# Kernel tuning notes

Measured on AMD Instinct MI355X. Metric: run time of the kernel, lower is better.

## Reference

```python
import jax, jax.numpy as jnp
import numpy as np


def setup_inputs() -> dict:
    key = jax.random.key(0)
    ks = jax.random.split(key, 12)
    B, T, D, H = 256, 512, 128, 256
    s = 0.01
    inp = {
        "x": jax.random.normal(ks[0], (B, T, D), dtype=jnp.float32),
        "h_decay": jax.random.uniform(ks[1], (B, T), dtype=jnp.float32),
        "Wr": jax.random.normal(ks[2], (D, H), dtype=jnp.float32) * s,
        "Wz": jax.random.normal(ks[3], (D, H), dtype=jnp.float32) * s,
        "Wh": jax.random.normal(ks[4], (D, H), dtype=jnp.float32) * s,
        "Ur": jax.random.normal(ks[5], (H, H), dtype=jnp.float32) * s,
        "Uz": jax.random.normal(ks[6], (H, H), dtype=jnp.float32) * s,
        "Uh": jax.random.normal(ks[7], (H, H), dtype=jnp.float32) * s,
        "br": jax.random.normal(ks[8], (H,), dtype=jnp.float32) * s,
        "bz": jax.random.normal(ks[9], (H,), dtype=jnp.float32) * s,
        "bh": jax.random.normal(ks[10], (H,), dtype=jnp.float32) * s,
    }
    return inp


def reference(x, h_decay, Wr, Wz, Wh, Ur, Uz, Uh, br, bz, bh):
    B, T, D = x.shape
    H = Ur.shape[0]
    # Precompute input projections for all timesteps (same math, batched GEMM).
    xz = jnp.einsum("btd,dh->bth", x, Wz) + bz  # [B,T,H]
    xr = jnp.einsum("btd,dh->bth", x, Wr) + br
    xh = jnp.einsum("btd,dh->bth", x, Wh) + bh

    def step(h_tm1, inputs):
        xz_t, xr_t, xh_t, dec_t = inputs
        h_dec = dec_t[:, None] * h_tm1              # decay previous state
        z_t = jax.nn.sigmoid(xz_t + h_dec @ Uz)
        r_t = jax.nn.sigmoid(xr_t + h_dec @ Ur)
        h_prop = jnp.tanh(xh_t + (r_t * h_dec) @ Uh)
        h_t = (1.0 - z_t) * h_dec + z_t * h_prop
        return h_t, h_t

    h0 = jnp.zeros((B, H), dtype=x.dtype)
    scan_inputs = (
        jnp.swapaxes(xz, 0, 1),  # [T,B,H]
        jnp.swapaxes(xr, 0, 1),
        jnp.swapaxes(xh, 0, 1),
        jnp.swapaxes(h_decay, 0, 1),  # [T,B]
    )
    _, hs = jax.lax.scan(step, h0, scan_inputs)
    return jnp.swapaxes(hs, 0, 1)  # [B,T,H]
```

## Files before the change

### kernel.cpp

```cpp
#include <hip/hip_runtime.h>
#include <hip/hip_bf16.h>


static constexpr int Bb = 256;
static constexpr int Tt = 512;
static constexpr int Dd = 128;
static constexpr int Hh = 256;

typedef _Float16 half2_t __attribute__((ext_vector_type(2)));

__device__ __forceinline__ float dot2f(unsigned a, unsigned b, float c) {
  half2_t av, bv;
  __builtin_memcpy(&av, &a, 4);
  __builtin_memcpy(&bv, &b, 4);
#if __has_builtin(__builtin_amdgcn_fdot2)
  return __builtin_amdgcn_fdot2(av, bv, c, false);
#else
  return fmaf((float)av[1], (float)bv[1], fmaf((float)av[0], (float)bv[0], c));
#endif
}

__device__ __forceinline__ unsigned packh2(float lo, float hi) {
  half2_t hv;
  hv[0] = (_Float16)lo;
  hv[1] = (_Float16)hi;
  unsigned u;
  __builtin_memcpy(&u, &hv, 4);
  return u;
}

__global__ __launch_bounds__(256) void proj3_kernel(
    const float* __restrict__ x,
    const float* __restrict__ Wz, const float* __restrict__ Wr,
    const float* __restrict__ Wh,
    const float* __restrict__ bz, const float* __restrict__ br,
    const float* __restrict__ bh,
    float* __restrict__ oz, float* __restrict__ orr, float* __restrict__ oh)
{
  __shared__ unsigned xP[64][64];
  __shared__ unsigned wP[8][256];

  const int tid = threadIdx.x;
  const int ty = tid >> 5;
  const int tx = tid & 31;
  const size_t brow = (size_t)blockIdx.x * 64;

  #pragma unroll
  for (int it = 0; it < 8; ++it) {
    int idx = it * 256 + tid;
    int row = idx & 63;
    int kq  = idx >> 6;
    float4 v = *(const float4*)(x + (brow + row) * Dd + kq * 4);
    xP[kq * 2 + 0][row] = packh2(v.x, v.y);
    xP[kq * 2 + 1][row] = packh2(v.z, v.w);
  }

  const float* Ws[3] = {Wz, Wr, Wh};
  const float* bs[3] = {bz, br, bh};
  float* os[3] = {oz, orr, oh};

  __syncthreads();

  for (int g = 0; g < 3; ++g) {
    float bv[8];
    *(float4*)&bv[0] = *(const float4*)(bs[g] + tx * 8);
    *(float4*)&bv[4] = *(const float4*)(bs[g] + tx * 8 + 4);

    float acc[8][8];
    #pragma unroll
    for (int i = 0; i < 8; ++i)
      #pragma unroll
      for (int jj = 0; jj < 8; ++jj) acc[i][jj] = 0.f;

    for (int s = 0; s < 8; ++s) {
      #pragma unroll
      for (int it = 0; it < 2; ++it) {
        int qq  = it * 256 + tid;
        int kkp = qq >> 6;
        int c4  = (qq & 63) * 4;
        const float* wr0 = Ws[g] + (size_t)((s * 8 + kkp) * 2) * Hh + c4;
        float4 wa = *(const float4*)wr0;
        float4 wb = *(const float4*)(wr0 + Hh);
        uint4 pk;
        pk.x = packh2(wa.x, wb.x);
        pk.y = packh2(wa.y, wb.y);
        pk.z = packh2(wa.z, wb.z);
        pk.w = packh2(wa.w, wb.w);
        *(uint4*)&wP[kkp][c4] = pk;
      }
      __syncthreads();

      #pragma unroll
      for (int kkp = 0; kkp < 8; ++kkp) {
        unsigned xv[8], wv[8];
        *(uint4*)&xv[0] = *(const uint4*)&xP[s * 8 + kkp][ty * 8];
        *(uint4*)&xv[4] = *(const uint4*)&xP[s * 8 + kkp][ty * 8 + 4];
        *(uint4*)&wv[0] = *(const uint4*)&wP[kkp][tx * 8];
        *(uint4*)&wv[4] = *(const uint4*)&wP[kkp][tx * 8 + 4];
        #pragma unroll
        for (int i = 0; i < 8; ++i)
          #pragma unroll
          for (int jj = 0; jj < 8; ++jj)
            acc[i][jj] = dot2f(xv[i], wv[jj], acc[i][jj]);
      }
      __syncthreads();
    }

    float* of = os[g];
    #pragma unroll
    for (int i = 0; i < 8; ++i) {
      size_t ro = (brow + (size_t)ty * 8 + i) * Hh + tx * 8;
      float4 a{acc[i][0] + bv[0], acc[i][1] + bv[1],
               acc[i][2] + bv[2], acc[i][3] + bv[3]};
      float4 c{acc[i][4] + bv[4], acc[i][5] + bv[5],
               acc[i][6] + bv[6], acc[i][7] + bv[7]};
      *(float4*)(of + ro) = a;
      *(float4*)(of + ro + 4) = c;
    }
  }
}

__global__ __launch_bounds__(768, 3) void gru_scan_g3(
    const float* __restrict__ xz, const float* __restrict__ xr,
    const float* __restrict__ hdecay,
    const float* __restrict__ Uz, const float* __restrict__ Ur,
    const float* __restrict__ Uh, float* __restrict__ out)
{
  const int tid = threadIdx.x;
  const int j   = tid & 255;
  const int g   = tid >> 8;
  const int b   = blockIdx.x;

  __shared__ unsigned hdp[128];
  __shared__ unsigned rhp[128];
  __shared__ float    zbuf[256];

  const float* Ug = (g == 0) ? Uz : (g == 1) ? Ur : Uh;
  unsigned uu[128];
  #pragma unroll
  for (int m = 0; m < 128; ++m)
    uu[m] = packh2(Ug[(size_t)(2 * m) * Hh + j],
                   Ug[(size_t)(2 * m + 1) * Hh + j]);

  if (tid < 128) hdp[tid] = 0u;

  const size_t bbase = (size_t)b * Tt * Hh;
  const int    hbase = b * Tt;

  float hd = 0.f;
  float xc = 0.f, xn = 0.f;
  float dec_n = 0.f, dec_n2 = 0.f;

  if (g == 0)      xc = xz[bbase + j];
  else if (g == 1) xc = xr[bbase + j];
  else { xc = out[bbase + j]; dec_n = hdecay[hbase + 1]; }
  __syncthreads();

  for (int t = 0; t < Tt; ++t) {
    {
      const int tp = (t + 1 < Tt) ? t + 1 : Tt - 1;
      const size_t bp = bbase + (size_t)tp * Hh + j;
      if (g == 0)      xn = xz[bp];
      else if (g == 1) xn = xr[bp];
      else {
        xn = out[bp];
        dec_n2 = hdecay[hbase + ((t + 2 < Tt) ? t + 2 : Tt - 1)];
      }
    }

    if (g < 2) {
      float acc[4] = {0.f, 0.f, 0.f, 0.f};
      #pragma unroll
      for (int u4 = 0; u4 < 32; ++u4) {
        uint4 hp4 = *(const uint4*)&hdp[u4 * 4];
        const int mb = u4 * 4;
        float a = acc[u4 & 3];
        a = dot2f(hp4.x, uu[mb + 0], a);
        a = dot2f(hp4.y, uu[mb + 1], a);
        a = dot2f(hp4.z, uu[mb + 2], a);
        a = dot2f(hp4.w, uu[mb + 3], a);
        acc[u4 & 3] = a;
      }
      float s = (acc[0] + acc[1]) + (acc[2] + acc[3]);
      if (g == 0) {
        zbuf[j] = 1.f / (1.f + __expf(-(xc + s)));
      } else {
        float rv = 1.f / (1.f + __expf(-(xc + s)));
        unsigned hp2 = hdp[j >> 1];
        half2_t hh;
        __builtin_memcpy(&hh, &hp2, 4);
        float rh = rv * (float)hh[j & 1];
        float nb = __shfl_xor(rh, 1, 64);
        if ((j & 1) == 0) rhp[j >> 1] = packh2(rh, nb);
      }
    }
    __syncthreads();

    if (g == 2) {
      float acc[4] = {0.f, 0.f, 0.f, 0.f};
      #pragma unroll
      for (int u4 = 0; u4 < 32; ++u4) {
        uint4 rp4 = *(const uint4*)&rhp[u4 * 4];
        const int mb = u4 * 4;
        float a = acc[u4 & 3];
        a = dot2f(rp4.x, uu[mb + 0], a);
        a = dot2f(rp4.y, uu[mb + 1], a);
        a = dot2f(rp4.z, uu[mb + 2], a);
        a = dot2f(rp4.w, uu[mb + 3], a);
        acc[u4 & 3] = a;
      }
      float s  = (acc[0] + acc[1]) + (acc[2] + acc[3]);
      float hs = xc + s;
      float ex = __expf(2.f * hs);
      float hp = 1.f - 2.f / (ex + 1.f);
      float zv = zbuf[j];
      float hn = (1.f - zv) * hd + zv * hp;
      out[bbase + (size_t)t * Hh + j] = hn;
      hd = dec_n * hn;
      float nb = __shfl_xor(hd, 1, 64);
      if ((j & 1) == 0) hdp[j >> 1] = packh2(hd, nb);
    }
    __syncthreads();

    xc = xn;
    dec_n = dec_n2;
  }
}

extern "C" void kernel_launch(void* const* d_in, const int* in_sizes, int n_in,
                              void* d_out, int out_size, void* d_ws, size_t ws_size,
                              hipStream_t stream) {
  const float* x   = (const float*)d_in[0];
  const float* hdc = (const float*)d_in[1];
  const float* Wr  = (const float*)d_in[2];
  const float* Wz  = (const float*)d_in[3];
  const float* Wh  = (const float*)d_in[4];
  const float* Ur  = (const float*)d_in[5];
  const float* Uz  = (const float*)d_in[6];
  const float* Uh  = (const float*)d_in[7];
  const float* br  = (const float*)d_in[8];
  const float* bz  = (const float*)d_in[9];
  const float* bh  = (const float*)d_in[10];
  float* out = (float*)d_out;

  const size_t bth = (size_t)Bb * Tt * Hh;
  float* wsz = (float*)d_ws;
  float* wsr = wsz + bth;

  proj3_kernel<<<dim3(2048), dim3(256), 0, stream>>>(
      x, Wz, Wr, Wh, bz, br, bh, wsz, wsr, out);

  gru_scan_g3<<<dim3(Bb), dim3(768), 0, stream>>>(
      wsz, wsr, hdc, Uz, Ur, Uh, out);
}
```

Baseline: 1.367 ms.

## Split GRU scan K-dimension across four lane quarters with shuffle reduction

The recurrent scan kernel now uses 1024 threads per batch row instead of three gate groups of 256. Each thread holds a quarter of the K range for all three U matrices and reduces partial sums with cross-lane shuffles. This shortens each thread's serial dot-product chain and lets the z and r gates share the hidden-state loads. The costs are extra shuffle reductions, redundant loads of xz, xr and xh across the four quarters, and a larger block that may limit occupancy.

```diff
diff --git a/kernel.cpp b/kernel.cpp
--- a/kernel.cpp
+++ b/kernel.cpp
@@ -120,110 +120,112 @@
   }
 }
 
-__global__ __launch_bounds__(768, 3) void gru_scan_g3(
+__global__ __launch_bounds__(1024, 4) void gru_scan_q4(
     const float* __restrict__ xz, const float* __restrict__ xr,
     const float* __restrict__ hdecay,
     const float* __restrict__ Uz, const float* __restrict__ Ur,
     const float* __restrict__ Uh, float* __restrict__ out)
 {
-  const int tid = threadIdx.x;
-  const int j   = tid & 255;
-  const int g   = tid >> 8;
-  const int b   = blockIdx.x;
+  const int tid  = threadIdx.x;
+  const int w    = tid >> 6;
+  const int lane = tid & 63;
+  const int q    = lane >> 4;
+  const int i    = lane & 15;
+  const int j    = w * 16 + i;
+  const int b    = blockIdx.x;
 
   __shared__ unsigned hdp[128];
   __shared__ unsigned rhp[128];
-  __shared__ float    zbuf[256];
-
-  const float* Ug = (g == 0) ? Uz : (g == 1) ? Ur : Uh;
-  unsigned uu[128];
-  #pragma unroll
-  for (int m = 0; m < 128; ++m)
-    uu[m] = packh2(Ug[(size_t)(2 * m) * Hh + j],
-                   Ug[(size_t)(2 * m + 1) * Hh + j]);
+
+  unsigned uz[32], ur[32], uh[32];
+  {
+    const int kb = q * 64;
+    const float* uzp = Uz + (size_t)kb * Hh + j;
+    const float* urp = Ur + (size_t)kb * Hh + j;
+    const float* uhp = Uh + (size_t)kb * Hh + j;
+    #pragma unroll
+    for (int m = 0; m < 32; ++m) {
+      uz[m] = packh2(uzp[(size_t)(2 * m) * Hh], uzp[(size_t)(2 * m + 1) * Hh]);
+      ur[m] = packh2(urp[(size_t)(2 * m) * Hh], urp[(size_t)(2 * m + 1) * Hh]);
+      uh[m] = packh2(uhp[(size_t)(2 * m) * Hh], uhp[(size_t)(2 * m + 1) * Hh]);
+    }
+  }
 
   if (tid < 128) hdp[tid] = 0u;
 
   const size_t bbase = (size_t)b * Tt * Hh;
   const int    hbase = b * Tt;
+  const float* pxz = xz + bbase + j;
+  const float* pxr = xr + bbase + j;
+  float*       pxh = out + bbase + j;
 
   float hd = 0.f;
-  float xc = 0.f, xn = 0.f;
-  float dec_n = 0.f, dec_n2 = 0.f;
-
-  if (g == 0)      xc = xz[bbase + j];
-  else if (g == 1) xc = xr[bbase + j];
-  else { xc = out[bbase + j]; dec_n = hdecay[hbase + 1]; }
+  float xz_c = pxz[0];
+  float xr_c = pxr[0];
+  float xh_c = pxh[0];
+  float dec_n = hdecay[hbase + 1];
   __syncthreads();
 
   for (int t = 0; t < Tt; ++t) {
-    {
-      const int tp = (t + 1 < Tt) ? t + 1 : Tt - 1;
-      const size_t bp = bbase + (size_t)tp * Hh + j;
-      if (g == 0)      xn = xz[bp];
-      else if (g == 1) xn = xr[bp];
-      else {
-        xn = out[bp];
-        dec_n2 = hdecay[hbase + ((t + 2 < Tt) ? t + 2 : Tt - 1)];
-      }
-    }
-
-    if (g < 2) {
-      float acc[4] = {0.f, 0.f, 0.f, 0.f};
-      #pragma unroll
-      for (int u4 = 0; u4 < 32; ++u4) {
-        uint4 hp4 = *(const uint4*)&hdp[u4 * 4];
-        const int mb = u4 * 4;
-        float a = acc[u4 & 3];
-        a = dot2f(hp4.x, uu[mb + 0], a);
-        a = dot2f(hp4.y, uu[mb + 1], a);
-        a = dot2f(hp4.z, uu[mb + 2], a);
-        a = dot2f(hp4.w, uu[mb + 3], a);
-        acc[u4 & 3] = a;
-      }
-      float s = (acc[0] + acc[1]) + (acc[2] + acc[3]);
-      if (g == 0) {
-        zbuf[j] = 1.f / (1.f + __expf(-(xc + s)));
-      } else {
-        float rv = 1.f / (1.f + __expf(-(xc + s)));
-        unsigned hp2 = hdp[j >> 1];
-        half2_t hh;
-        __builtin_memcpy(&hh, &hp2, 4);
-        float rh = rv * (float)hh[j & 1];
-        float nb = __shfl_xor(rh, 1, 64);
-        if ((j & 1) == 0) rhp[j >> 1] = packh2(rh, nb);
-      }
-    }
+    const int tp = (t + 1 < Tt) ? t + 1 : Tt - 1;
+    const int to = tp * Hh;
+    float xz_n = pxz[to];
+    float xr_n = pxr[to];
+    float xh_n = pxh[to];
+    float dec_n2 = hdecay[hbase + ((t + 2 < Tt) ? t + 2 : Tt - 1)];
+
+    float az0 = 0.f, az1 = 0.f, ar0 = 0.f, ar1 = 0.f;
+    #pragma unroll
+    for (int m8 = 0; m8 < 8; ++m8) {
+      uint4 hp4 = *(const uint4*)&hdp[q * 32 + m8 * 4];
+      const int mb = m8 * 4;
+      az0 = dot2f(hp4.x, uz[mb + 0], az0);
+      az1 = dot2f(hp4.y, uz[mb + 1], az1);
+      az0 = dot2f(hp4.z, uz[mb + 2], az0);
+      az1 = dot2f(hp4.w, uz[mb + 3], az1);
+      ar0 = dot2f(hp4.x, ur[mb + 0], ar0);
+      ar1 = dot2f(hp4.y, ur[mb + 1], ar1);
+      ar0 = dot2f(hp4.z, ur[mb + 2], ar0);
+      ar1 = dot2f(hp4.w, ur[mb + 3], ar1);
+    }
+    float sz = az0 + az1;
+    float sr = ar0 + ar1;
+    sz += __shfl_xor(sz, 16, 64);
+    sz += __shfl_xor(sz, 32, 64);
+    sr += __shfl_xor(sr, 16, 64);
+    sr += __shfl_xor(sr, 32, 64);
+    const float zv = 1.f / (1.f + __expf(-(xz_c + sz)));
+    const float rv = 1.f / (1.f + __expf(-(xr_c + sr)));
+    float rh = rv * hd;
+    float nbr = __shfl_xor(rh, 1, 64);
+    if (q == 0 && (i & 1) == 0)
+      rhp[w * 8 + (i >> 1)] = packh2(rh, nbr);
     __syncthreads();
 
-    if (g == 2) {
-      float acc[4] = {0.f, 0.f, 0.f, 0.f};
-      #pragma unroll
-      for (int u4 = 0; u4 < 32; ++u4) {
-        uint4 rp4 = *(const uint4*)&rhp[u4 * 4];
-        const int mb = u4 * 4;
-        float a = acc[u4 & 3];
-        a = dot2f(rp4.x, uu[mb + 0], a);
-        a = dot2f(rp4.y, uu[mb + 1], a);
-        a = dot2f(rp4.z, uu[mb + 2], a);
-        a = dot2f(rp4.w, uu[mb + 3], a);
-        acc[u4 & 3] = a;
-      }
-      float s  = (acc[0] + acc[1]) + (acc[2] + acc[3]);
-      float hs = xc + s;
-      float ex = __expf(2.f * hs);
-      float hp = 1.f - 2.f / (ex + 1.f);
-      float zv = zbuf[j];
-      float hn = (1.f - zv) * hd + zv * hp;
-      out[bbase + (size_t)t * Hh + j] = hn;
-      hd = dec_n * hn;
-      float nb = __shfl_xor(hd, 1, 64);
-      if ((j & 1) == 0) hdp[j >> 1] = packh2(hd, nb);
-    }
+    float ah0 = 0.f, ah1 = 0.f;
+    #pragma unroll
+    for (int m8 = 0; m8 < 8; ++m8) {
+      uint4 rp4 = *(const uint4*)&rhp[q * 32 + m8 * 4];
+      const int mb = m8 * 4;
+      ah0 = dot2f(rp4.x, uh[mb + 0], ah0);
+      ah1 = dot2f(rp4.y, uh[mb + 1], ah1);
+      ah0 = dot2f(rp4.z, uh[mb + 2], ah0);
+      ah1 = dot2f(rp4.w, uh[mb + 3], ah1);
+    }
+    float sh = ah0 + ah1;
+    sh += __shfl_xor(sh, 16, 64);
+    sh += __shfl_xor(sh, 32, 64);
+    const float hs = xh_c + sh;
+    const float ex = __expf(2.f * hs);
+    const float hp = 1.f - 2.f / (ex + 1.f);
+    const float hn = (1.f - zv) * hd + zv * hp;
+    if (q == 0) pxh[t * Hh] = hn;
+    hd = dec_n * hn;
+    float nbh = __shfl_xor(hd, 1, 64);
+    if (q == 0 && (i & 1) == 0)
+      hdp[w * 8 + (i >> 1)] = packh2(hd, nbh);
+    xz_c = xz_n; xr_c = xr_n; xh_c = xh_n; dec_n = dec_n2;
     __syncthreads();
-
-    xc = xn;
-    dec_n = dec_n2;
   }
 }
 
@@ -250,6 +252,6 @@
   proj3_kernel<<<dim3(2048), dim3(256), 0, stream>>>(
       x, Wz, Wr, Wh, bz, br, bh, wsz, wsr, out);
 
-  gru_scan_g3<<<dim3(Bb), dim3(768), 0, stream>>>(
+  gru_scan_q4<<<dim3(Bb), dim3(1024), 0, stream>>>(
       wsz, wsr, hdc, Uz, Ur, Uh, out);
 }
```

Result: slower. 1.468 ms (+7.4%).
